# Optimization experiments

Hardware: AMD Instinct MI355X
Metric: run time of the kernel (lower is better)

The kernel has to match this reference:

```python
import jax, jax.numpy as jnp
import numpy as np

# Static config (from MSDeformAttnPixelDecoder defaults, 1024x1024 input, strides 8/16/32 reversed)
SHAPES = [(32, 32), (64, 64), (128, 128)]  # (H, W) per level, order as fed to the transformer
B, C, NH, NL, NP, NLAYERS, DFF = 4, 256, 8, 3, 4, 6, 1024
HD = C // NH
S = sum(h * w for h, w in SHAPES)
STARTS = np.concatenate([[0], np.cumsum([h * w for h, w in SHAPES])[:-1]]).tolist()


def setup_inputs() -> dict:
    key = jax.random.key(0)
    ks = jax.random.split(key, 24)
    def nrm(k, shape, scale):
        return jax.random.normal(k, shape, jnp.float32) * scale
    inp = {}
    for i, (h, w) in enumerate(SHAPES):
        inp[f'src{i}'] = jax.random.normal(ks[i], (B, C, h, w), jnp.float32)
        inp[f'pos{i}'] = jax.random.normal(ks[3 + i], (B, C, h, w), jnp.float32)
    L = NLAYERS
    inp['level_embed'] = nrm(ks[6], (NL, C), 1.0)
    inp['Wv'] = nrm(ks[7], (L, C, C), 0.02); inp['bv'] = jnp.zeros((L, C), jnp.float32)
    inp['Wo'] = nrm(ks[8], (L, C, NH * NL * NP * 2), 0.01)
    inp['bo'] = nrm(ks[9], (L, NH * NL * NP * 2), 0.5)  # stands in for the grid-init offset bias
    inp['Wa'] = nrm(ks[10], (L, C, NH * NL * NP), 0.02); inp['ba'] = jnp.zeros((L, NH * NL * NP), jnp.float32)
    inp['Wout'] = nrm(ks[11], (L, C, C), 0.02); inp['bout'] = jnp.zeros((L, C), jnp.float32)
    inp['ln1_g'] = jnp.ones((L, C), jnp.float32); inp['ln1_b'] = jnp.zeros((L, C), jnp.float32)
    inp['W1'] = nrm(ks[12], (L, C, DFF), 0.02); inp['b1'] = jnp.zeros((L, DFF), jnp.float32)
    inp['W2'] = nrm(ks[13], (L, DFF, C), 0.02); inp['b2'] = jnp.zeros((L, C), jnp.float32)
    inp['ln2_g'] = jnp.ones((L, C), jnp.float32); inp['ln2_b'] = jnp.zeros((L, C), jnp.float32)
    return inp


def _layer_norm(x, g, b):
    m = x.mean(-1, keepdims=True)
    v = ((x - m) ** 2).mean(-1, keepdims=True)
    return (x - m) * jax.lax.rsqrt(v + 1e-5) * g + b


def _bilinear_sample(v, loc):
    # v: [BH, Hl, Wl, D]; loc: [BH, P, 2] normalized (x, y) in [0,1].
    # Matches F.grid_sample(mode=bilinear, padding_mode=zeros, align_corners=False)
    BH, Hl, Wl, D = v.shape
    x = loc[..., 0] * Wl - 0.5
    y = loc[..., 1] * Hl - 0.5
    x0f = jnp.floor(x); y0f = jnp.floor(y)
    lx = x - x0f; ly = y - y0f
    x0 = x0f.astype(jnp.int32); y0 = y0f.astype(jnp.int32)
    bidx = jnp.arange(BH)[:, None]
    def g(yi, xi):
        valid = (xi >= 0) & (xi < Wl) & (yi >= 0) & (yi < Hl)
        vi = v[bidx, jnp.clip(yi, 0, Hl - 1), jnp.clip(xi, 0, Wl - 1)]
        return jnp.where(valid[..., None], vi, 0.0)
    v00 = g(y0, x0); v01 = g(y0, x0 + 1); v10 = g(y0 + 1, x0); v11 = g(y0 + 1, x0 + 1)
    wx0 = 1.0 - lx; wy0 = 1.0 - ly
    return (v00 * (wx0 * wy0)[..., None] + v01 * (lx * wy0)[..., None]
            + v10 * (wx0 * ly)[..., None] + v11 * (lx * ly)[..., None])


def _forward(src0, src1, src2, pos0, pos1, pos2, level_embed,
             Wv, bv, Wo, bo, Wa, ba, Wout, bout, ln1_g, ln1_b,
             W1, b1, W2, b2, ln2_g, ln2_b):
    srcs, poss = [src0, src1, src2], [pos0, pos1, pos2]
    # Flatten [B,C,H,W] -> [B,HW,C], add level embedding to pos
    src = jnp.concatenate([s.reshape(B, C, -1).transpose(0, 2, 1) for s in srcs], axis=1)
    pos = jnp.concatenate([
        p.reshape(B, C, -1).transpose(0, 2, 1) + level_embed[i][None, None, :]
        for i, p in enumerate(poss)], axis=1)
    # Reference points: pixel centers, normalized; valid_ratios == 1 (masks all False)
    refs = []
    for h, w in SHAPES:
        ry = (jnp.arange(h, dtype=jnp.float32) + 0.5) / h
        rx = (jnp.arange(w, dtype=jnp.float32) + 0.5) / w
        gy, gx = jnp.meshgrid(ry, rx, indexing='ij')
        refs.append(jnp.stack([gx.reshape(-1), gy.reshape(-1)], -1))
    ref = jnp.concatenate(refs, 0)  # [S, 2] (x, y); same for every level since valid_ratios=1
    wh = jnp.array([[w, h] for h, w in SHAPES], jnp.float32)  # [NL, 2] (W, H)

    output = src
    for l in range(NLAYERS):
        q = output + pos
        value = (output @ Wv[l] + bv[l]).reshape(B, S, NH, HD)
        offs = (q @ Wo[l] + bo[l]).reshape(B, S, NH, NL, NP, 2)
        aw = jax.nn.softmax((q @ Wa[l] + ba[l]).reshape(B, S, NH, NL * NP), axis=-1)
        aw = aw.reshape(B, S, NH, NL, NP)
        loc = ref[None, :, None, None, None, :] + offs / wh[None, None, None, :, None, :]
        attn = jnp.zeros((B, S, NH, HD), output.dtype)
        for lvl, (h, w) in enumerate(SHAPES):
            s0 = STARTS[lvl]
            v_l = value[:, s0:s0 + h * w].transpose(0, 2, 1, 3).reshape(B * NH, h, w, HD)
            loc_l = loc[:, :, :, lvl].transpose(0, 2, 1, 3, 4).reshape(B * NH, S * NP, 2)
            samp = _bilinear_sample(v_l, loc_l).reshape(B, NH, S, NP, HD)
            attn = attn + jnp.einsum('bhspd,bshp->bshd', samp, aw[:, :, :, lvl])
        attn_out = attn.reshape(B, S, C) @ Wout[l] + bout[l]
        output = _layer_norm(output + attn_out, ln1_g[l], ln1_b[l])
        ff = jax.nn.relu(output @ W1[l] + b1[l]) @ W2[l] + b2[l]
        output = _layer_norm(output + ff, ln2_g[l], ln2_b[l])
    return output  # [B, S, C] encoder memory


def reference(src0, src1, src2, pos0, pos1, pos2, level_embed,
              Wv, bv, Wo, bo, Wa, ba, Wout, bout, ln1_g, ln1_b,
              W1, b1, W2, b2, ln2_g, ln2_b):
    return _forward(src0, src1, src2, pos0, pos1, pos2, level_embed,
                    Wv, bv, Wo, bo, Wa, ba, Wout, bout, ln1_g, ln1_b,
                    W1, b1, W2, b2, ln2_g, ln2_b)
```

## Files before the change

### kernel.cpp

```cpp
#include <hip/hip_runtime.h>
#include <stdint.h>

#define S_TOT 21504
#define M_TOK 86016

typedef __attribute__((ext_vector_type(8))) short bf16x8;
typedef __attribute__((ext_vector_type(4))) float f32x4;
typedef __attribute__((ext_vector_type(2))) float f32x2;

__device__ __forceinline__ unsigned short f2b(float f) {
  union { float f; unsigned u; } v; v.f = f;
  unsigned r = v.u + 0x7FFFu + ((v.u >> 16) & 1u);
  return (unsigned short)(r >> 16);
}
__device__ __forceinline__ float b2f(unsigned short h) {
  union { unsigned u; float f; } v; v.u = ((unsigned)h) << 16;
  return v.f;
}
__device__ __forceinline__ float blo(unsigned u) {
  union { unsigned u; float f; } v; v.u = u << 16; return v.f;
}
__device__ __forceinline__ float bhi(unsigned u) {
  union { unsigned u; float f; } v; v.u = u & 0xffff0000u; return v.f;
}
__device__ __forceinline__ f32x2 unpk(unsigned u) {
  union { unsigned u; float f; } lo, hi;
  lo.u = u << 16; hi.u = u & 0xffff0000u;
  return (f32x2){lo.f, hi.f};
}

#define LSTR 40
template <int RELU>
__global__ __launch_bounds__(256) void gemm_kernel(
    const unsigned short* __restrict__ A, const unsigned short* __restrict__ Bt,
    const float* __restrict__ bias, const float* __restrict__ bias2, int nsplit,
    unsigned short* __restrict__ C, int N, int K) {
  __shared__ unsigned short Alds[128 * LSTR];
  __shared__ unsigned short Blds[128 * LSTR];
  const int tid = threadIdx.x;
  const int wave = tid >> 6, lane = tid & 63;
  const long m0 = (long)blockIdx.y * 128;
  const int n0 = blockIdx.x * 128;
  const int wm = (wave >> 1) * 64, wn = (wave & 1) * 64;

  f32x4 acc[4][4];
#pragma unroll
  for (int i = 0; i < 4; i++)
#pragma unroll
    for (int j = 0; j < 4; j++) acc[i][j] = (f32x4){0.f, 0.f, 0.f, 0.f};

  const int ar = tid >> 2, ak = (tid & 3) * 8;
  int brA = n0 + ar;      if (brA >= N) brA = N - 1;
  int brB = n0 + ar + 64; if (brB >= N) brB = N - 1;
  const unsigned short* a0p = A + (m0 + ar) * (long)K + ak;
  const unsigned short* a1p = A + (m0 + ar + 64) * (long)K + ak;
  const unsigned short* b0p = Bt + (long)brA * K + ak;
  const unsigned short* b1p = Bt + (long)brB * K + ak;
  unsigned short* aw0 = Alds + ar * LSTR + ak;
  unsigned short* aw1 = Alds + (ar + 64) * LSTR + ak;
  unsigned short* bw0 = Blds + ar * LSTR + ak;
  unsigned short* bw1 = Blds + (ar + 64) * LSTR + ak;

  uint4 a0 = *(const uint4*)a0p;
  uint4 a1 = *(const uint4*)a1p;
  uint4 b0 = *(const uint4*)b0p;
  uint4 b1 = *(const uint4*)b1p;

  for (int k0 = 0; k0 < K; k0 += 32) {
    if (k0) __syncthreads();
    *(uint4*)aw0 = a0;
    *(uint4*)aw1 = a1;
    *(uint4*)bw0 = b0;
    *(uint4*)bw1 = b1;
    if (k0 + 32 < K) {
      a0 = *(const uint4*)(a0p + k0 + 32);
      a1 = *(const uint4*)(a1p + k0 + 32);
      b0 = *(const uint4*)(b0p + k0 + 32);
      b1 = *(const uint4*)(b1p + k0 + 32);
    }
    __syncthreads();

    const int kk = (lane >> 4) * 8;
    bf16x8 af[4], bq[4];
#pragma unroll
    for (int i = 0; i < 4; i++)
      af[i] = *(const bf16x8*)&Alds[(wm + i * 16 + (lane & 15)) * LSTR + kk];
#pragma unroll
    for (int j = 0; j < 4; j++)
      bq[j] = *(const bf16x8*)&Blds[(wn + j * 16 + (lane & 15)) * LSTR + kk];
#pragma unroll
    for (int i = 0; i < 4; i++)
#pragma unroll
      for (int j = 0; j < 4; j++)
        acc[i][j] = __builtin_amdgcn_mfma_f32_16x16x32_bf16(af[i], bq[j], acc[i][j], 0, 0, 0);
  }

  unsigned short* stage = Alds;
  const int colb = lane & 15, rowb = (lane >> 4) * 4;
#pragma unroll
  for (int half = 0; half < 2; half++) {
    __syncthreads();
    if (wm == half * 64) {
#pragma unroll
      for (int j = 0; j < 4; j++) {
        const int n = n0 + wn + j * 16 + colb;
        const float bn = (n < N) ? ((n < nsplit) ? bias[n] : bias2[n - nsplit]) : 0.f;
#pragma unroll
        for (int i = 0; i < 4; i++) {
#pragma unroll
          for (int r = 0; r < 4; r++) {
            float v = acc[i][j][r] + bn;
            if (RELU) v = fmaxf(v, 0.f);
            stage[(i * 16 + rowb + r) * 136 + wn + j * 16 + colb] = f2b(v);
          }
        }
      }
    }
    __syncthreads();
#pragma unroll
    for (int t = 0; t < 4; t++) {
      const int idx = t * 256 + tid;
      const int rr = idx >> 4;
      const int cc = (idx & 15) * 8;
      const int n = n0 + cc;
      if (n < N) {
        const long m = m0 + half * 64 + rr;
        *(uint4*)(C + m * N + n) = *(const uint4*)(stage + rr * 136 + cc);
      }
    }
  }
}

__global__ void wtrans_kernel(const float* __restrict__ src, unsigned short* __restrict__ dst,
                              int K, int N, size_t src_lstride, size_t dst_lstride) {
  __shared__ float t[32][33];
  const int tx = threadIdx.x, ty = threadIdx.y;
  const int n0 = blockIdx.x * 32, k0 = blockIdx.y * 32, l = blockIdx.z;
  src += (size_t)l * src_lstride;
  dst += (size_t)l * dst_lstride;
#pragma unroll
  for (int i = 0; i < 4; i++) t[ty * 4 + i][tx] = src[(size_t)(k0 + ty * 4 + i) * N + n0 + tx];
  __syncthreads();
#pragma unroll
  for (int i = 0; i < 4; i++)
    dst[(size_t)(n0 + ty * 4 + i) * K + k0 + tx] = f2b(t[tx][ty * 4 + i]);
}

__global__ void flatten_kernel(const float* __restrict__ src, const float* __restrict__ pos,
                               const float* __restrict__ lemb,
                               unsigned short* __restrict__ outb, unsigned short* __restrict__ posb,
                               unsigned short* __restrict__ qb, int HW, int s0) {
  __shared__ float ts[32][33];
  __shared__ float tp[32][33];
  const int tx = threadIdx.x, ty = threadIdx.y;
  const int hw0 = blockIdx.x * 32, c0 = blockIdx.y * 32, b = blockIdx.z;
  const size_t ibase = ((size_t)b * 256 + c0) * HW + hw0;
#pragma unroll
  for (int i = 0; i < 4; i++) {
    ts[ty * 4 + i][tx] = src[ibase + (size_t)(ty * 4 + i) * HW + tx];
    tp[ty * 4 + i][tx] = pos[ibase + (size_t)(ty * 4 + i) * HW + tx];
  }
  __syncthreads();
#pragma unroll
  for (int i = 0; i < 4; i++) {
    const int sI = s0 + hw0 + ty * 4 + i, c = c0 + tx;
    const size_t o = ((size_t)b * S_TOT + sI) * 256 + c;
    const float sv = ts[tx][ty * 4 + i];
    const unsigned short pb = f2b(tp[tx][ty * 4 + i] + lemb[c]);
    outb[o] = f2b(sv);
    posb[o] = pb;
    qb[o] = f2b(sv + b2f(pb));
  }
}

__global__ __launch_bounds__(256) void deform_kernel(const unsigned short* __restrict__ value,
                                                     const unsigned short* __restrict__ oa,
                                                     unsigned short* __restrict__ attn) {
  __shared__ float law[4][96];
  __shared__ uint4 didx[4][96];
  __shared__ float4 dwt[4][96];
  const int tid = threadIdx.x;
  const int wv = tid >> 6, lane = tid & 63;
  const int bs = blockIdx.x * 4 + wv;
  const int b = bs / S_TOT, s = bs - b * S_TOT;

  if (lane < 8) {
    const unsigned short* ap = oa + (size_t)bs * 288 + 192 + lane * 12;
    const uint2 p0 = *(const uint2*)ap;
    const uint2 p1 = *(const uint2*)(ap + 4);
    const uint2 p2 = *(const uint2*)(ap + 8);
    float a[12] = {blo(p0.x), bhi(p0.x), blo(p0.y), bhi(p0.y),
                   blo(p1.x), bhi(p1.x), blo(p1.y), bhi(p1.y),
                   blo(p2.x), bhi(p2.x), blo(p2.y), bhi(p2.y)};
    float mx = a[0];
#pragma unroll
    for (int i = 1; i < 12; i++) mx = fmaxf(mx, a[i]);
    float e[12], sm = 0.f;
#pragma unroll
    for (int i = 0; i < 12; i++) { e[i] = __expf(a[i] - mx); sm += e[i]; }
    const float r = 1.f / sm;
#pragma unroll
    for (int i = 0; i < 12; i++) law[wv][lane * 12 + i] = e[i] * r;
  }
  __syncthreads();

  float rx, ry;
  {
    if (s < 1024) { const int li = s; rx = ((li & 31) + 0.5f) * (1.f / 32); ry = ((li >> 5) + 0.5f) * (1.f / 32); }
    else if (s < 5120) { const int li = s - 1024; rx = ((li & 63) + 0.5f) * (1.f / 64); ry = ((li >> 6) + 0.5f) * (1.f / 64); }
    else { const int li = s - 5120; rx = ((li & 127) + 0.5f) * (1.f / 128); ry = ((li >> 7) + 0.5f) * (1.f / 128); }
  }

  for (int ti = lane; ti < 96; ti += 64) {
    const int h = ti / 12;
    const int rem = ti - h * 12;
    const int lvl = rem >> 2;
    const int wl = 32 << lvl;
    const float fwl = (float)wl;
    const int start = (lvl == 0) ? 0 : ((lvl == 1) ? 1024 : 5120);
    const unsigned op = *(const unsigned*)(oa + (size_t)bs * 288 + 2 * ti);
    const float ox = blo(op), oy = bhi(op);
    const float x = (rx + ox / fwl) * fwl - 0.5f;
    const float y = (ry + oy / fwl) * fwl - 0.5f;
    const float xf = floorf(x), yf = floorf(y);
    const int x0 = (int)xf, y0 = (int)yf;
    const float fx = x - xf, fy = y - yf;
    const bool xv0 = (x0 >= 0) & (x0 < wl), xv1 = (x0 + 1 >= 0) & (x0 + 1 < wl);
    const bool yv0 = (y0 >= 0) & (y0 < wl), yv1 = (y0 + 1 >= 0) & (y0 + 1 < wl);
    const int x0c = min(max(x0, 0), wl - 1), x1c = min(max(x0 + 1, 0), wl - 1);
    const int y0c = min(max(y0, 0), wl - 1), y1c = min(max(y0 + 1, 0), wl - 1);
    const float w = law[wv][ti];
    float4 w4;
    w4.x = (xv0 & yv0) ? w * (1.f - fx) * (1.f - fy) : 0.f;
    w4.y = (xv1 & yv0) ? w * fx * (1.f - fy) : 0.f;
    w4.z = (xv0 & yv1) ? w * (1.f - fx) * fy : 0.f;
    w4.w = (xv1 & yv1) ? w * fx * fy : 0.f;
    const unsigned base = (unsigned)(((b * S_TOT + start) << 8) + h * 32) * 2u;
    uint4 iv;
    iv.x = base + (unsigned)(y0c * wl + x0c) * 512u;
    iv.y = base + (unsigned)(y0c * wl + x1c) * 512u;
    iv.z = base + (unsigned)(y1c * wl + x0c) * 512u;
    iv.w = base + (unsigned)(y1c * wl + x1c) * 512u;
    didx[wv][ti] = iv;
    dwt[wv][ti] = w4;
  }
  __syncthreads();

  const int h = lane >> 3, c = (lane & 7) * 4;
  const char* vb = (const char*)value + c * 2;
  const uint4* ip = &didx[wv][h * 12];
  const float4* wp = &dwt[wv][h * 12];
  f32x2 acc0 = (f32x2){0.f, 0.f}, acc1 = (f32x2){0.f, 0.f};
#pragma unroll
  for (int t = 0; t < 12; t++) {
    const uint4 iv = ip[t];
    const float4 w4 = wp[t];
    const uint2 q00 = *(const uint2*)(vb + iv.x);
    const uint2 q01 = *(const uint2*)(vb + iv.y);
    const uint2 q10 = *(const uint2*)(vb + iv.z);
    const uint2 q11 = *(const uint2*)(vb + iv.w);
    const f32x2 w0 = (f32x2){w4.x, w4.x}, w1 = (f32x2){w4.y, w4.y};
    const f32x2 w2 = (f32x2){w4.z, w4.z}, w3 = (f32x2){w4.w, w4.w};
    acc0 += w0 * unpk(q00.x) + w1 * unpk(q01.x) + w2 * unpk(q10.x) + w3 * unpk(q11.x);
    acc1 += w0 * unpk(q00.y) + w1 * unpk(q01.y) + w2 * unpk(q10.y) + w3 * unpk(q11.y);
  }
  uint2 o;
  o.x = (unsigned)f2b(acc0.x) | ((unsigned)f2b(acc0.y) << 16);
  o.y = (unsigned)f2b(acc1.x) | ((unsigned)f2b(acc1.y) << 16);
  *(uint2*)(attn + (size_t)bs * 256 + h * 32 + c) = o;
}

__global__ __launch_bounds__(256) void resln_kernel(const unsigned short* __restrict__ x,
                                                    const unsigned short* __restrict__ r,
                                                    const float* __restrict__ g,
                                                    const float* __restrict__ bta,
                                                    unsigned short* __restrict__ ob,
                                                    const unsigned short* __restrict__ pos,
                                                    unsigned short* __restrict__ qb,
                                                    float* __restrict__ fout) {
  const int t = blockIdx.x * 4 + (threadIdx.x >> 6);
  const int lane = threadIdx.x & 63;
  const size_t base = (size_t)t * 256;
  const ushort4 xv = ((const ushort4*)(x + base))[lane];
  const ushort4 rv = ((const ushort4*)(r + base))[lane];
  const float v0 = b2f(xv.x) + b2f(rv.x), v1 = b2f(xv.y) + b2f(rv.y);
  const float v2 = b2f(xv.z) + b2f(rv.z), v3 = b2f(xv.w) + b2f(rv.w);
  float sm = v0 + v1 + v2 + v3;
#pragma unroll
  for (int o = 32; o > 0; o >>= 1) sm += __shfl_xor(sm, o);
  const float mean = sm * (1.f / 256.f);
  const float d0 = v0 - mean, d1 = v1 - mean, d2 = v2 - mean, d3 = v3 - mean;
  float vs = d0 * d0 + d1 * d1 + d2 * d2 + d3 * d3;
#pragma unroll
  for (int o = 32; o > 0; o >>= 1) vs += __shfl_xor(vs, o);
  const float inv = rsqrtf(vs * (1.f / 256.f) + 1e-5f);
  const int c = lane * 4;
  const float o0 = d0 * inv * g[c] + bta[c];
  const float o1 = d1 * inv * g[c + 1] + bta[c + 1];
  const float o2 = d2 * inv * g[c + 2] + bta[c + 2];
  const float o3 = d3 * inv * g[c + 3] + bta[c + 3];
  if (fout) {
    ((float4*)(fout + base))[lane] = make_float4(o0, o1, o2, o3);
  } else {
    ushort4 u;
    u.x = f2b(o0); u.y = f2b(o1); u.z = f2b(o2); u.w = f2b(o3);
    ((ushort4*)(ob + base))[lane] = u;
  }
  if (qb) {
    const ushort4 pv = ((const ushort4*)(pos + base))[lane];
    ushort4 u;
    u.x = f2b(o0 + b2f(pv.x)); u.y = f2b(o1 + b2f(pv.y));
    u.z = f2b(o2 + b2f(pv.z)); u.w = f2b(o3 + b2f(pv.w));
    ((ushort4*)(qb + base))[lane] = u;
  }
}

extern "C" void kernel_launch(void* const* d_in, const int* in_sizes, int n_in,
                              void* d_out, int out_size, void* d_ws, size_t ws_size,
                              hipStream_t stream) {
  (void)in_sizes; (void)n_in; (void)out_size;
  const float* src0 = (const float*)d_in[0];
  const float* pos0 = (const float*)d_in[1];
  const float* src1 = (const float*)d_in[2];
  const float* pos1 = (const float*)d_in[3];
  const float* src2 = (const float*)d_in[4];
  const float* pos2 = (const float*)d_in[5];
  const float* lemb = (const float*)d_in[6];
  const float* Wv = (const float*)d_in[7];   const float* bv = (const float*)d_in[8];
  const float* Wo = (const float*)d_in[9];   const float* bo = (const float*)d_in[10];
  const float* Wa = (const float*)d_in[11];  const float* ba = (const float*)d_in[12];
  const float* Wout = (const float*)d_in[13]; const float* bout = (const float*)d_in[14];
  const float* ln1g = (const float*)d_in[15]; const float* ln1b = (const float*)d_in[16];
  const float* W1 = (const float*)d_in[17];  const float* b1 = (const float*)d_in[18];
  const float* W2 = (const float*)d_in[19];  const float* b2 = (const float*)d_in[20];
  const float* ln2g = (const float*)d_in[21]; const float* ln2b = (const float*)d_in[22];

  const size_t M = M_TOK;
  const size_t SZ16 = 44040192ull;
  const size_t POOL = 176160768ull;
  const size_t NEED = SZ16 + POOL + SZ16 + SZ16 + 8749056ull;
  if (ws_size < NEED) return;

  char* ws = (char*)d_ws;
  unsigned short* slot0b = (unsigned short*)ws;
  unsigned short* valb = slot0b;
  unsigned short* woutb = slot0b;
  unsigned short* ffb = slot0b;
  char* pool = ws + SZ16;
  unsigned short* q_b16 = (unsigned short*)pool;
  unsigned short* oa_b16 = (unsigned short*)pool + M * 256;
  unsigned short* attn_b16 = (unsigned short*)pool + M * 544;
  unsigned short* h_b16 = (unsigned short*)pool;
  unsigned short* out_b16 = (unsigned short*)(pool + POOL);
  unsigned short* pos_b16 = out_b16 + M * 256;
  unsigned short* wt = pos_b16 + M * 256;

  unsigned short* wtv = wt;
  unsigned short* wtoa = wt + 393216;
  unsigned short* wtw = wt + 835584;
  unsigned short* wt1 = wt + 1228800;
  unsigned short* wt2 = wt + 2801664;

  const dim3 b32(32, 8);
  wtrans_kernel<<<dim3(8, 8, 6), b32, 0, stream>>>(Wv, wtv, 256, 256, 65536, 65536);
  wtrans_kernel<<<dim3(6, 8, 6), b32, 0, stream>>>(Wo, wtoa, 256, 192, 49152, 73728);
  wtrans_kernel<<<dim3(3, 8, 6), b32, 0, stream>>>(Wa, wtoa + 192 * 256, 256, 96, 24576, 73728);
  wtrans_kernel<<<dim3(8, 8, 6), b32, 0, stream>>>(Wout, wtw, 256, 256, 65536, 65536);
  wtrans_kernel<<<dim3(32, 8, 6), b32, 0, stream>>>(W1, wt1, 256, 1024, 262144, 262144);
  wtrans_kernel<<<dim3(8, 32, 6), b32, 0, stream>>>(W2, wt2, 1024, 256, 262144, 262144);

  flatten_kernel<<<dim3(32, 8, 4), b32, 0, stream>>>(src0, pos0, lemb, out_b16, pos_b16, q_b16, 1024, 0);
  flatten_kernel<<<dim3(128, 8, 4), b32, 0, stream>>>(src1, pos1, lemb + 256, out_b16, pos_b16, q_b16, 4096, 1024);
  flatten_kernel<<<dim3(512, 8, 4), b32, 0, stream>>>(src2, pos2, lemb + 512, out_b16, pos_b16, q_b16, 16384, 5120);

  for (int l = 0; l < 6; l++) {
    gemm_kernel<0><<<dim3(2, 672), 256, 0, stream>>>(out_b16, wtv + l * 65536, bv + l * 256, bv + l * 256, 256, valb, 256, 256);
    gemm_kernel<0><<<dim3(3, 672), 256, 0, stream>>>(q_b16, wtoa + l * 73728, bo + l * 192, ba + l * 96, 192, oa_b16, 288, 256);
    deform_kernel<<<21504, 256, 0, stream>>>(valb, oa_b16, attn_b16);
    gemm_kernel<0><<<dim3(2, 672), 256, 0, stream>>>(attn_b16, wtw + l * 65536, bout + l * 256, bout + l * 256, 256, woutb, 256, 256);
    resln_kernel<<<21504, 256, 0, stream>>>(out_b16, woutb, ln1g + l * 256, ln1b + l * 256, out_b16, nullptr, nullptr, nullptr);
    gemm_kernel<1><<<dim3(8, 672), 256, 0, stream>>>(out_b16, wt1 + l * 262144, b1 + l * 1024, b1 + l * 1024, 1024, h_b16, 1024, 256);
    gemm_kernel<0><<<dim3(2, 672), 256, 0, stream>>>(h_b16, wt2 + l * 262144, b2 + l * 256, b2 + l * 256, 256, ffb, 256, 1024);
    if (l < 5) {
      resln_kernel<<<21504, 256, 0, stream>>>(out_b16, ffb, ln2g + l * 256, ln2b + l * 256, out_b16, pos_b16, q_b16, nullptr);
    } else {
      resln_kernel<<<21504, 256, 0, stream>>>(out_b16, ffb, ln2g + l * 256, ln2b + l * 256, nullptr, nullptr, nullptr, (float*)d_out);
    }
  }
}
```

Before: 2.811 ms.

## Fuse output-projection and FFN2 GEMMs with residual LayerNorm epilogue

Adds a GEMM kernel with 64-row by full-256-column tiles that stages the biased result in shared memory, then does the residual add and LayerNorm, plus the optional pos-add query output, in the same block. It replaces the Wout GEMM plus resln and the W2 GEMM plus resln pairs, removing the bf16 intermediate write and read and two launches per layer. In exchange the tile shape changes from 128x128 to 64x256 and the grid shrinks to 1344 blocks, which may affect MFMA efficiency and occupancy. The epilogue LayerNorm runs row-serial across waves.

```diff
diff --git a/kernel.cpp b/kernel.cpp
--- a/kernel.cpp
+++ b/kernel.cpp
@@ -30,6 +30,7 @@
 }
 
 #define LSTR 40
+
 template <int RELU>
 __global__ __launch_bounds__(256) void gemm_kernel(
     const unsigned short* __restrict__ A, const unsigned short* __restrict__ Bt,
@@ -127,6 +128,131 @@
         const long m = m0 + half * 64 + rr;
         *(uint4*)(C + m * N + n) = *(const uint4*)(stage + rr * 136 + cc);
       }
+    }
+  }
+}
+
+__global__ __launch_bounds__(256) void gemm_ln_kernel(
+    const unsigned short* __restrict__ A, const unsigned short* __restrict__ Bt,
+    const float* __restrict__ bias, const unsigned short* __restrict__ x,
+    const float* __restrict__ g, const float* __restrict__ bta,
+    unsigned short* __restrict__ ob, const unsigned short* __restrict__ pos,
+    unsigned short* __restrict__ qb, float* __restrict__ fout, int K) {
+  __shared__ unsigned short smem[64 * 264];
+  unsigned short* Alds = smem;
+  unsigned short* Blds = smem + 64 * LSTR;
+  const int tid = threadIdx.x;
+  const int wave = tid >> 6, lane = tid & 63;
+  const long m0 = (long)blockIdx.x * 64;
+  const int wm = (wave >> 1) * 32, wn = (wave & 1) * 128;
+  const int l15 = lane & 15, lhi = lane >> 4;
+
+  f32x4 acc[2][8];
+#pragma unroll
+  for (int i = 0; i < 2; i++)
+#pragma unroll
+    for (int j = 0; j < 8; j++) acc[i][j] = (f32x4){0.f, 0.f, 0.f, 0.f};
+
+  const int srow = tid >> 2, sk = (tid & 3) * 8;
+  const unsigned short* apA = A + (m0 + srow) * (long)K + sk;
+  const unsigned short* bp0 = Bt + (long)srow * K + sk;
+  const unsigned short* bp1 = Bt + (long)(srow + 64) * K + sk;
+  const unsigned short* bp2 = Bt + (long)(srow + 128) * K + sk;
+  const unsigned short* bp3 = Bt + (long)(srow + 192) * K + sk;
+  unsigned short* awp = Alds + srow * LSTR + sk;
+  unsigned short* bwp0 = Blds + srow * LSTR + sk;
+  unsigned short* bwp1 = Blds + (srow + 64) * LSTR + sk;
+  unsigned short* bwp2 = Blds + (srow + 128) * LSTR + sk;
+  unsigned short* bwp3 = Blds + (srow + 192) * LSTR + sk;
+
+  uint4 ra = *(const uint4*)apA;
+  uint4 rb0 = *(const uint4*)bp0;
+  uint4 rb1 = *(const uint4*)bp1;
+  uint4 rb2 = *(const uint4*)bp2;
+  uint4 rb3 = *(const uint4*)bp3;
+
+  for (int k0 = 0; k0 < K; k0 += 32) {
+    if (k0) __syncthreads();
+    *(uint4*)awp = ra;
+    *(uint4*)bwp0 = rb0;
+    *(uint4*)bwp1 = rb1;
+    *(uint4*)bwp2 = rb2;
+    *(uint4*)bwp3 = rb3;
+    if (k0 + 32 < K) {
+      ra = *(const uint4*)(apA + k0 + 32);
+      rb0 = *(const uint4*)(bp0 + k0 + 32);
+      rb1 = *(const uint4*)(bp1 + k0 + 32);
+      rb2 = *(const uint4*)(bp2 + k0 + 32);
+      rb3 = *(const uint4*)(bp3 + k0 + 32);
+    }
+    __syncthreads();
+
+    const int kk = lhi * 8;
+    bf16x8 af[2], bq[8];
+#pragma unroll
+    for (int i = 0; i < 2; i++)
+      af[i] = *(const bf16x8*)&Alds[(wm + i * 16 + l15) * LSTR + kk];
+#pragma unroll
+    for (int j = 0; j < 8; j++)
+      bq[j] = *(const bf16x8*)&Blds[(wn + j * 16 + l15) * LSTR + kk];
+#pragma unroll
+    for (int i = 0; i < 2; i++)
+#pragma unroll
+      for (int j = 0; j < 8; j++)
+        acc[i][j] = __builtin_amdgcn_mfma_f32_16x16x32_bf16(af[i], bq[j], acc[i][j], 0, 0, 0);
+  }
+
+  __syncthreads();
+  {
+    const int rowb = lhi * 4;
+#pragma unroll
+    for (int j = 0; j < 8; j++) {
+      const int n = wn + j * 16 + l15;
+      const float bn = bias[n];
+#pragma unroll
+      for (int i = 0; i < 2; i++)
+#pragma unroll
+        for (int r = 0; r < 4; r++)
+          smem[(wm + i * 16 + rowb + r) * 264 + n] = f2b(acc[i][j][r] + bn);
+    }
+  }
+  __syncthreads();
+
+  for (int rr = 0; rr < 16; rr++) {
+    const int row = wave * 16 + rr;
+    const long m = m0 + row;
+    const size_t base = (size_t)m * 256;
+    const ushort4 xv = *(const ushort4*)(x + base + lane * 4);
+    const ushort4 rv = *(const ushort4*)(smem + row * 264 + lane * 4);
+    const float v0 = b2f(xv.x) + b2f(rv.x), v1 = b2f(xv.y) + b2f(rv.y);
+    const float v2 = b2f(xv.z) + b2f(rv.z), v3 = b2f(xv.w) + b2f(rv.w);
+    float sm = v0 + v1 + v2 + v3;
+#pragma unroll
+    for (int o = 32; o > 0; o >>= 1) sm += __shfl_xor(sm, o);
+    const float mean = sm * (1.f / 256.f);
+    const float d0 = v0 - mean, d1 = v1 - mean, d2 = v2 - mean, d3 = v3 - mean;
+    float vs = d0 * d0 + d1 * d1 + d2 * d2 + d3 * d3;
+#pragma unroll
+    for (int o = 32; o > 0; o >>= 1) vs += __shfl_xor(vs, o);
+    const float inv = rsqrtf(vs * (1.f / 256.f) + 1e-5f);
+    const int c = lane * 4;
+    const float o0 = d0 * inv * g[c] + bta[c];
+    const float o1 = d1 * inv * g[c + 1] + bta[c + 1];
+    const float o2 = d2 * inv * g[c + 2] + bta[c + 2];
+    const float o3 = d3 * inv * g[c + 3] + bta[c + 3];
+    if (fout) {
+      ((float4*)(fout + base))[lane] = make_float4(o0, o1, o2, o3);
+    } else {
+      ushort4 u;
+      u.x = f2b(o0); u.y = f2b(o1); u.z = f2b(o2); u.w = f2b(o3);
+      ((ushort4*)(ob + base))[lane] = u;
+    }
+    if (qb) {
+      const ushort4 pv = ((const ushort4*)(pos + base))[lane];
+      ushort4 u;
+      u.x = f2b(o0 + b2f(pv.x)); u.y = f2b(o1 + b2f(pv.y));
+      u.z = f2b(o2 + b2f(pv.z)); u.w = f2b(o3 + b2f(pv.w));
+      ((ushort4*)(qb + base))[lane] = u;
     }
   }
 }
@@ -270,51 +396,6 @@
   *(uint2*)(attn + (size_t)bs * 256 + h * 32 + c) = o;
 }
 
-__global__ __launch_bounds__(256) void resln_kernel(const unsigned short* __restrict__ x,
-                                                    const unsigned short* __restrict__ r,
-                                                    const float* __restrict__ g,
-                                                    const float* __restrict__ bta,
-                                                    unsigned short* __restrict__ ob,
-                                                    const unsigned short* __restrict__ pos,
-                                                    unsigned short* __restrict__ qb,
-                                                    float* __restrict__ fout) {
-  const int t = blockIdx.x * 4 + (threadIdx.x >> 6);
-  const int lane = threadIdx.x & 63;
-  const size_t base = (size_t)t * 256;
-  const ushort4 xv = ((const ushort4*)(x + base))[lane];
-  const ushort4 rv = ((const ushort4*)(r + base))[lane];
-  const float v0 = b2f(xv.x) + b2f(rv.x), v1 = b2f(xv.y) + b2f(rv.y);
-  const float v2 = b2f(xv.z) + b2f(rv.z), v3 = b2f(xv.w) + b2f(rv.w);
-  float sm = v0 + v1 + v2 + v3;
-#pragma unroll
-  for (int o = 32; o > 0; o >>= 1) sm += __shfl_xor(sm, o);
-  const float mean = sm * (1.f / 256.f);
-  const float d0 = v0 - mean, d1 = v1 - mean, d2 = v2 - mean, d3 = v3 - mean;
-  float vs = d0 * d0 + d1 * d1 + d2 * d2 + d3 * d3;
-#pragma unroll
-  for (int o = 32; o > 0; o >>= 1) vs += __shfl_xor(vs, o);
-  const float inv = rsqrtf(vs * (1.f / 256.f) + 1e-5f);
-  const int c = lane * 4;
-  const float o0 = d0 * inv * g[c] + bta[c];
-  const float o1 = d1 * inv * g[c + 1] + bta[c + 1];
-  const float o2 = d2 * inv * g[c + 2] + bta[c + 2];
-  const float o3 = d3 * inv * g[c + 3] + bta[c + 3];
-  if (fout) {
-    ((float4*)(fout + base))[lane] = make_float4(o0, o1, o2, o3);
-  } else {
-    ushort4 u;
-    u.x = f2b(o0); u.y = f2b(o1); u.z = f2b(o2); u.w = f2b(o3);
-    ((ushort4*)(ob + base))[lane] = u;
-  }
-  if (qb) {
-    const ushort4 pv = ((const ushort4*)(pos + base))[lane];
-    ushort4 u;
-    u.x = f2b(o0 + b2f(pv.x)); u.y = f2b(o1 + b2f(pv.y));
-    u.z = f2b(o2 + b2f(pv.z)); u.w = f2b(o3 + b2f(pv.w));
-    ((ushort4*)(qb + base))[lane] = u;
-  }
-}
-
 extern "C" void kernel_launch(void* const* d_in, const int* in_sizes, int n_in,
                               void* d_out, int out_size, void* d_ws, size_t ws_size,
                               hipStream_t stream) {
@@ -342,10 +423,7 @@
   if (ws_size < NEED) return;
 
   char* ws = (char*)d_ws;
-  unsigned short* slot0b = (unsigned short*)ws;
-  unsigned short* valb = slot0b;
-  unsigned short* woutb = slot0b;
-  unsigned short* ffb = slot0b;
+  unsigned short* valb = (unsigned short*)ws;
   char* pool = ws + SZ16;
   unsigned short* q_b16 = (unsigned short*)pool;
   unsigned short* oa_b16 = (unsigned short*)pool + M * 256;
@@ -377,14 +455,18 @@
     gemm_kernel<0><<<dim3(2, 672), 256, 0, stream>>>(out_b16, wtv + l * 65536, bv + l * 256, bv + l * 256, 256, valb, 256, 256);
     gemm_kernel<0><<<dim3(3, 672), 256, 0, stream>>>(q_b16, wtoa + l * 73728, bo + l * 192, ba + l * 96, 192, oa_b16, 288, 256);
     deform_kernel<<<21504, 256, 0, stream>>>(valb, oa_b16, attn_b16);
-    gemm_kernel<0><<<dim3(2, 672), 256, 0, stream>>>(attn_b16, wtw + l * 65536, bout + l * 256, bout + l * 256, 256, woutb, 256, 256);
-    resln_kernel<<<21504, 256, 0, stream>>>(out_b16, woutb, ln1g + l * 256, ln1b + l * 256, out_b16, nullptr, nullptr, nullptr);
+    gemm_ln_kernel<<<1344, 256, 0, stream>>>(attn_b16, wtw + l * 65536, bout + l * 256, out_b16,
+                                             ln1g + l * 256, ln1b + l * 256, out_b16,
+                                             nullptr, nullptr, nullptr, 256);
     gemm_kernel<1><<<dim3(8, 672), 256, 0, stream>>>(out_b16, wt1 + l * 262144, b1 + l * 1024, b1 + l * 1024, 1024, h_b16, 1024, 256);
-    gemm_kernel<0><<<dim3(2, 672), 256, 0, stream>>>(h_b16, wt2 + l * 262144, b2 + l * 256, b2 + l * 256, 256, ffb, 256, 1024);
     if (l < 5) {
-      resln_kernel<<<21504, 256, 0, stream>>>(out_b16, ffb, ln2g + l * 256, ln2b + l * 256, out_b16, pos_b16, q_b16, nullptr);
+      gemm_ln_kernel<<<1344, 256, 0, stream>>>(h_b16, wt2 + l * 262144, b2 + l * 256, out_b16,
+                                               ln2g + l * 256, ln2b + l * 256, out_b16,
+                                               pos_b16, q_b16, nullptr, 1024);
     } else {
-      resln_kernel<<<21504, 256, 0, stream>>>(out_b16, ffb, ln2g + l * 256, ln2b + l * 256, nullptr, nullptr, nullptr, (float*)d_out);
-    }
-  }
-}
+      gemm_ln_kernel<<<1344, 256, 0, stream>>>(h_b16, wt2 + l * 262144, b2 + l * 256, out_b16,
+                                               ln2g + l * 256, ln2b + l * 256, nullptr,
+                                               nullptr, nullptr, (float*)d_out, 1024);
+    }
+  }
+}
```

Result: slower. 2.943 ms (+4.7%).
